# Kernel tuning notes

Measured on AMD Instinct MI355X. Metric: run time of the kernel, lower is better.

Reference implementation:

```python
import jax, jax.numpy as jnp
import numpy as np

THETA = 1.0       # spiking threshold (params['neuron']['theta'])
TAU_SR = 10.0     # SRM synaptic time constant (tauSr)
K = 100           # srm kernel support; alpha kernel has decayed to ~0 by 10*tau


def srm_kernel():
    # SLAYER SRMALPHA kernel: eps(t) = (t/tau) * exp(1 - t/tau), t = 0..K-1 (Ts = 1)
    t = jnp.arange(K, dtype=jnp.float32)
    return (t / TAU_SR) * jnp.exp(1.0 - t / TAU_SR)


def psp(x):
    # Causal temporal convolution with shared SRM kernel: y[t] = sum_s eps[s] * x[t-s]
    # x: [B, C, T]
    B, C, T = x.shape
    k = srm_kernel()[::-1].reshape(1, 1, K)  # flip: lax conv is correlation
    xr = x.reshape(B * C, 1, T)
    y = jax.lax.conv_general_dilated(xr, k, window_strides=(1,), padding=[(K - 1, 0)])
    return y.reshape(B, C, T)


def spike(u):
    # Hard threshold (forward of SLAYER spike function)
    return (u >= THETA).astype(u.dtype)


def setup_inputs() -> dict:
    key = jax.random.key(0)
    k1, k2, k3 = jax.random.split(key, 3)
    B, T = 256, 1000
    IN, HID, OUT = 78, 16, 20
    spike_input = (jax.random.uniform(k1, (B, IN, T)) < 0.1).astype(jnp.float32)
    W1 = jax.random.normal(k2, (HID, IN), dtype=jnp.float32) * 0.3
    W2 = jax.random.normal(k3, (OUT, HID), dtype=jnp.float32) * 0.3
    return {"spike_input": spike_input, "W1": W1, "W2": W2}


def reference(spike_input, W1, W2):
    # layer 1: dense (per-timestep matmul) -> psp temporal filter -> spike threshold
    u1 = psp(jnp.einsum('hi,bit->bht', W1, spike_input))  # [B, HID, T]
    s1 = spike(u1)
    # layer 2
    u2 = psp(jnp.einsum('oh,bht->bot', W2, s1))           # [B, OUT, T]
    return spike(u2)
```

## Files before the change

kernel.cpp:

```cpp
#include <hip/hip_runtime.h>
#include <math.h>


#define B_     256
#define IN_    78
#define HID_   16
#define OUT_   20
#define T_     1000
#define TT_    125
#define J_     224
#define ZSTR_  228
#define TC_    128
#define MSTR_  132

#define GRP(EP, A0,A1,A2,A3, B0,B1,B2,B3, C0,C1,C2) { \
  const double2 e01_ = *(const double2*)(EP); \
  const double2 e23_ = *(const double2*)((EP)+2); \
  u0 += e01_.x*(A3); u1 += e01_.x*(B0); u2 += e01_.x*(B1); u3 += e01_.x*(B2); \
  u4 += e01_.x*(B3); u5 += e01_.x*(C0); u6 += e01_.x*(C1); u7 += e01_.x*(C2); \
  u0 += e01_.y*(A2); u1 += e01_.y*(A3); u2 += e01_.y*(B0); u3 += e01_.y*(B1); \
  u4 += e01_.y*(B2); u5 += e01_.y*(B3); u6 += e01_.y*(C0); u7 += e01_.y*(C1); \
  u0 += e23_.x*(A1); u1 += e23_.x*(A2); u2 += e23_.x*(A3); u3 += e23_.x*(B0); \
  u4 += e23_.x*(B1); u5 += e23_.x*(B2); u6 += e23_.x*(B3); u7 += e23_.x*(C0); \
  u0 += e23_.y*(A0); u1 += e23_.y*(A1); u2 += e23_.y*(A2); u3 += e23_.y*(A3); \
  u4 += e23_.y*(B0); u5 += e23_.y*(B1); u6 += e23_.y*(B2); u7 += e23_.y*(B3); }

#define LOADF(X0,X1,X2,X3, P) { \
  const float4 lf_ = *(const float4*)(P); \
  X0 = (double)lf_.x; X1 = (double)lf_.y; X2 = (double)lf_.z; X3 = (double)lf_.w; }

__device__ __forceinline__ void init_eps_d(double* eps_d, int tid) {
  if (tid < 100) {
    float a = (float)tid / 10.0f;
    float e = a * expf(1.0f - a);
    eps_d[tid] = (double)e;
  }
}

#define MMROW2(XR, W0, W1) { \
  const float2 f0_ = *(const float2*)(XR); \
  const float2 f1_ = *(const float2*)((XR) + 64); \
  const double x0_=(double)f0_.x, x1_=(double)f0_.y; \
  const double x2_=(double)f1_.x, x3_=(double)f1_.y; \
  m00 += (W0)*x0_; m01 += (W0)*x1_; m02 += (W0)*x2_; m03 += (W0)*x3_; \
  m10 += (W1)*x0_; m11 += (W1)*x1_; m12 += (W1)*x2_; m13 += (W1)*x3_; }

#define STORE2(BASE, EOFF, MA, MB) \
  if (tb + (EOFF) < T_ - 1) \
    *(float2*)&zout[(BASE) + (size_t)(tb + (EOFF))] = \
        make_float2((float)(MA), (float)(MB));

__global__ __launch_bounds__(256) void mm1(
    const float* __restrict__ x, const float* __restrict__ W1,
    float* __restrict__ zout)
{
  __shared__ float  xs[13 * MSTR_];
  __shared__ double wd[16 * 80];

  const int tid = threadIdx.x;
  const int b   = blockIdx.x >> 3;
  const int tc  = blockIdx.x & 7;
  const int tcb = tc * TC_;

  for (int idx = tid; idx < HID_ * IN_; idx += 256)
    wd[(idx / IN_) * 80 + (idx % IN_)] = (double)W1[idx];

  const int  c_  = tid & 127;
  const int  r0_ = tid >> 7;
  const int  tg_ = tcb + c_;
  const bool tok = (tg_ < T_);
  const bool t6  = tok && (r0_ == 0);

  const int p = tid >> 5;
  const int q = tid & 31;

  double m00=0,m01=0,m02=0,m03=0,m10=0,m11=0,m12=0,m13=0;
  float g0,g1,g2,g3,g4,g5,g6;

#define ISSUE_MM1(CI) { \
    const float* xb_ = x + ((size_t)b * IN_ + (CI) * 13 + r0_) * T_ + tg_; \
    g0 = tok ? xb_[0]       : 0.0f; \
    g1 = tok ? xb_[2  * T_] : 0.0f; \
    g2 = tok ? xb_[4  * T_] : 0.0f; \
    g3 = tok ? xb_[6  * T_] : 0.0f; \
    g4 = tok ? xb_[8  * T_] : 0.0f; \
    g5 = tok ? xb_[10 * T_] : 0.0f; \
    g6 = t6  ? xb_[12 * T_] : 0.0f; }

  ISSUE_MM1(0)
  for (int ci = 0; ci < 6; ++ci) {
    __syncthreads();
    {
      float* dst = &xs[r0_ * MSTR_ + c_];
      dst[0]          = g0;  dst[2  * MSTR_] = g1;
      dst[4  * MSTR_] = g2;  dst[6  * MSTR_] = g3;
      dst[8  * MSTR_] = g4;  dst[10 * MSTR_] = g5;
      if (r0_ == 0) dst[12 * MSTR_] = g6;
    }
    __syncthreads();
    if (ci < 5) ISSUE_MM1(ci + 1)
    const int wbase0 = (2*p)     * 80 + ci * 13;
    const int wbase1 = (2*p + 1) * 80 + ci * 13;
#pragma unroll
    for (int i = 0; i < 13; ++i) {
      const float* xr = &xs[i * MSTR_ + 2 * q];
      MMROW2(xr, wd[wbase0 + i], wd[wbase1 + i])
    }
  }

  const size_t r0s = ((size_t)b * HID_ + 2*p) * T_;
  const size_t r1s = r0s + T_;
  const int tb = tcb + 2 * q;
  STORE2(r0s,  0, m00, m01)  STORE2(r0s, 64, m02, m03)
  STORE2(r1s,  0, m10, m11)  STORE2(r1s, 64, m12, m13)
}

__global__ __launch_bounds__(256) void mm2(
    const float* __restrict__ s1, const float* __restrict__ W2,
    float* __restrict__ zout)
{
  __shared__ float  ss[16 * MSTR_];
  __shared__ double wd[OUT_ * HID_];

  const int tid = threadIdx.x;
  const int b   = blockIdx.x >> 3;
  const int tc  = blockIdx.x & 7;
  const int tcb = tc * TC_;

  for (int idx = tid; idx < OUT_ * HID_; idx += 256)
    wd[idx] = (double)W2[idx];

  {
    const int  c_  = tid & 127;
    const int  r0_ = tid >> 7;
    const int  tg_ = tcb + c_;
    const bool tok = (tg_ < T_);
    const float* sb = s1 + ((size_t)b * HID_ + r0_) * T_ + tg_;
    float* dst = &ss[r0_ * MSTR_ + c_];
#pragma unroll
    for (int e = 0; e < 8; ++e)
      dst[2 * e * MSTR_] = tok ? sb[2 * e * T_] : 0.0f;
  }
  __syncthreads();

  const int p  = tid >> 5;
  const int q  = tid & 31;
  const int tb = tcb + 2 * q;

  for (int pg = p; pg < 10; pg += 8) {
    double m00=0,m01=0,m02=0,m03=0,m10=0,m11=0,m12=0,m13=0;
    const int wbase0 = (2*pg)     * HID_;
    const int wbase1 = (2*pg + 1) * HID_;
#pragma unroll
    for (int i = 0; i < HID_; ++i) {
      const float* xr = &ss[i * MSTR_ + 2 * q];
      MMROW2(xr, wd[wbase0 + i], wd[wbase1 + i])
    }
    const size_t r0s = ((size_t)b * OUT_ + 2*pg) * T_;
    const size_t r1s = r0s + T_;
    STORE2(r0s,  0, m00, m01)  STORE2(r0s, 64, m02, m03)
    STORE2(r1s,  0, m10, m11)  STORE2(r1s, 64, m12, m13)
  }
}

__global__ __launch_bounds__(256) void fir_g(
    const float* __restrict__ zin, float* __restrict__ sout,
    int R, int tile_fixed)
{
  __shared__ float zf[OUT_ * ZSTR_];
  __shared__ __align__(16) double eps_d[100];

  const int tid  = threadIdx.x;
  const int b    = (tile_fixed >= 0) ? (int)blockIdx.x : (int)(blockIdx.x >> 3);
  const int tile = (tile_fixed >= 0) ? tile_fixed      : (int)(blockIdx.x & 7);
  const int t0   = tile * TT_;

  init_eps_d(eps_d, tid);
  for (int idx = tid; idx < R * ZSTR_; idx += 256) {
    const int cc = idx % ZSTR_;
    const int t  = t0 - 99 + cc;
    const int r  = idx / ZSTR_;
    zf[idx] = (cc < J_ && t >= 0) ? zin[((size_t)b * R + r) * T_ + t] : 0.0f;
  }
  __syncthreads();

  for (int task = tid; task < R * 16; task += 256) {
    const int h = task >> 4, q = task & 15;
    const float* zrow = &zf[h * ZSTR_ + 8 * q];
    double u0=0,u1=0,u2=0,u3=0,u4=0,u5=0,u6=0,u7=0;
    double A0,A1,A2,A3,B0,B1,B2,B3,C0,C1,C2,C3;
    LOADF(A0,A1,A2,A3, zrow + 96);
    LOADF(B0,B1,B2,B3, zrow + 100);
    LOADF(C0,C1,C2,C3, zrow + 104);
    GRP(eps_d, A0,A1,A2,A3, B0,B1,B2,B3, C0,C1,C2)

    const float*  zp = zrow + 92;
    const double* ep = eps_d + 4;
#pragma unroll 1
    for (int k = 0; k < 8; ++k) {
      LOADF(C0,C1,C2,C3, zp);
      GRP(ep,     C0,C1,C2,C3, A0,A1,A2,A3, B0,B1,B2)
      LOADF(B0,B1,B2,B3, zp - 4);
      GRP(ep + 4, B0,B1,B2,B3, C0,C1,C2,C3, A0,A1,A2)
      LOADF(A0,A1,A2,A3, zp - 8);
      GRP(ep + 8, A0,A1,A2,A3, B0,B1,B2,B3, C0,C1,C2)
      zp -= 12; ep += 12;
    }

    const size_t base = ((size_t)b * R + h) * T_ + t0 + 8 * q;
    const int tb = 8 * q;
    const float f0=(float)u0, f1=(float)u1, f2=(float)u2, f3=(float)u3;
    const float f4=(float)u4, f5=(float)u5, f6=(float)u6, f7=(float)u7;
    sout[base + 0] = (f0 >= 1.0f) ? 1.0f : 0.0f;
    sout[base + 1] = (f1 >= 1.0f) ? 1.0f : 0.0f;
    sout[base + 2] = (f2 >= 1.0f) ? 1.0f : 0.0f;
    sout[base + 3] = (f3 >= 1.0f) ? 1.0f : 0.0f;
    if (tb + 4 < TT_) sout[base + 4] = (f4 >= 1.0f) ? 1.0f : 0.0f;
    if (tb + 5 < TT_) sout[base + 5] = (f5 >= 1.0f) ? 1.0f : 0.0f;
    if (tb + 6 < TT_) sout[base + 6] = (f6 >= 1.0f) ? 1.0f : 0.0f;
    if (tb + 7 < TT_) sout[base + 7] = (f7 >= 1.0f) ? 1.0f : 0.0f;
  }
}

extern "C" void kernel_launch(void* const* d_in, const int* in_sizes, int n_in,
                              void* d_out, int out_size, void* d_ws, size_t ws_size,
                              hipStream_t stream) {
  const float* x  = (const float*)d_in[0];
  const float* W1 = (const float*)d_in[1];
  const float* W2 = (const float*)d_in[2];
  float* outp = (float*)d_out;
  float* base = (float*)d_ws;

  const size_t Z1E = (size_t)B_ * HID_ * T_;
  const size_t Z2E = (size_t)B_ * OUT_ * T_;

  if (ws_size >= (Z1E + Z2E) * sizeof(float)) {
    float* z1 = base;
    float* s1 = base + Z2E;
    float* z2 = base;
    mm1<<<dim3(B_ * 8), dim3(256), 0, stream>>>(x, W1, z1);
    fir_g<<<dim3(B_ * 8), dim3(256), 0, stream>>>(z1, s1, HID_, -1);
    mm2<<<dim3(B_ * 8), dim3(256), 0, stream>>>(s1, W2, z2);
    fir_g<<<dim3(B_ * 8), dim3(256), 0, stream>>>(z2, outp, OUT_, -1);
  } else if (ws_size >= 2 * Z1E * sizeof(float)) {
    float* z1 = base;
    float* s1 = base + Z1E;
    mm1<<<dim3(B_ * 8), dim3(256), 0, stream>>>(x, W1, z1);
    fir_g<<<dim3(B_ * 8), dim3(256), 0, stream>>>(z1, s1, HID_, -1);
    mm2<<<dim3(B_ * 8), dim3(256), 0, stream>>>(s1, W2, outp);
    for (int k = 7; k >= 0; --k)
      fir_g<<<dim3(B_), dim3(256), 0, stream>>>(outp, outp, OUT_, k);
  } else {
    float* z1 = base;
    mm1<<<dim3(B_ * 8), dim3(256), 0, stream>>>(x, W1, z1);
    for (int k = 7; k >= 0; --k)
      fir_g<<<dim3(B_), dim3(256), 0, stream>>>(z1, z1, HID_, k);
    mm2<<<dim3(B_ * 8), dim3(256), 0, stream>>>(z1, W2, outp);
    for (int k = 7; k >= 0; --k)
      fir_g<<<dim3(B_), dim3(256), 0, stream>>>(outp, outp, OUT_, k);
  }
}
```

Before: 109.8 us.

## Fuse layer-1 FIR/threshold with layer-2 matmul into one kernel

Adds a kernel that loads a z1 time tile with halo into shared memory, runs the first PSP filter and threshold, keeps the s1 spikes in shared memory, and immediately does the W2 matmul to write z2. This removes one kernel launch and the global round trip of s1. The final FIR now runs with 320 threads so all 20 output rows times 16 tasks are covered in one pass, and z1 is staged in the output buffer to reduce workspace needs. The fused kernel carries larger shared memory, which may reduce occupancy.

```diff
diff --git a/kernel.cpp b/kernel.cpp
--- a/kernel.cpp
+++ b/kernel.cpp
@@ -28,6 +28,25 @@
 #define LOADF(X0,X1,X2,X3, P) { \
   const float4 lf_ = *(const float4*)(P); \
   X0 = (double)lf_.x; X1 = (double)lf_.y; X2 = (double)lf_.z; X3 = (double)lf_.w; }
+
+#define FIR_BODY(ZROW) { \
+  double A0,A1,A2,A3,B0,B1,B2,B3,C0,C1,C2,C3; \
+  LOADF(A0,A1,A2,A3, (ZROW) + 96); \
+  LOADF(B0,B1,B2,B3, (ZROW) + 100); \
+  LOADF(C0,C1,C2,C3, (ZROW) + 104); \
+  GRP(eps_d, A0,A1,A2,A3, B0,B1,B2,B3, C0,C1,C2) \
+  const float*  zp_ = (ZROW) + 92; \
+  const double* ep_ = eps_d + 4; \
+  _Pragma("unroll 1") \
+  for (int k_ = 0; k_ < 8; ++k_) { \
+    LOADF(C0,C1,C2,C3, zp_); \
+    GRP(ep_,     C0,C1,C2,C3, A0,A1,A2,A3, B0,B1,B2) \
+    LOADF(B0,B1,B2,B3, zp_ - 4); \
+    GRP(ep_ + 4, B0,B1,B2,B3, C0,C1,C2,C3, A0,A1,A2) \
+    LOADF(A0,A1,A2,A3, zp_ - 8); \
+    GRP(ep_ + 8, A0,A1,A2,A3, B0,B1,B2,B3, C0,C1,C2) \
+    zp_ -= 12; ep_ += 12; \
+  } }
 
 __device__ __forceinline__ void init_eps_d(double* eps_d, int tid) {
   if (tid < 100) {
@@ -115,55 +134,79 @@
   STORE2(r1s,  0, m10, m11)  STORE2(r1s, 64, m12, m13)
 }
 
-__global__ __launch_bounds__(256) void mm2(
-    const float* __restrict__ s1, const float* __restrict__ W2,
-    float* __restrict__ zout)
+__global__ __launch_bounds__(256) void fm(
+    const float* __restrict__ z1, const float* __restrict__ W2,
+    float* __restrict__ z2)
 {
-  __shared__ float  ss[16 * MSTR_];
-  __shared__ double wd[OUT_ * HID_];
-
-  const int tid = threadIdx.x;
-  const int b   = blockIdx.x >> 3;
-  const int tc  = blockIdx.x & 7;
-  const int tcb = tc * TC_;
-
+  __shared__ float zf[HID_ * ZSTR_];
+  __shared__ float sf[HID_ * 128];
+  __shared__ float wf[OUT_ * HID_];
+  __shared__ __align__(16) double eps_d[100];
+
+  const int tid  = threadIdx.x;
+  const int b    = blockIdx.x >> 3;
+  const int tile = blockIdx.x & 7;
+  const int t0   = tile * TT_;
+
+  init_eps_d(eps_d, tid);
   for (int idx = tid; idx < OUT_ * HID_; idx += 256)
-    wd[idx] = (double)W2[idx];
+    wf[idx] = W2[idx];
+  for (int idx = tid; idx < HID_ * ZSTR_; idx += 256) {
+    const int cc = idx % ZSTR_;
+    const int t  = t0 - 99 + cc;
+    const int r  = idx / ZSTR_;
+    zf[idx] = (cc < J_ && t >= 0) ? z1[((size_t)b * HID_ + r) * T_ + t] : 0.0f;
+  }
+  __syncthreads();
 
   {
-    const int  c_  = tid & 127;
-    const int  r0_ = tid >> 7;
-    const int  tg_ = tcb + c_;
-    const bool tok = (tg_ < T_);
-    const float* sb = s1 + ((size_t)b * HID_ + r0_) * T_ + tg_;
-    float* dst = &ss[r0_ * MSTR_ + c_];
+    const int h = tid >> 4, q16 = tid & 15;
+    const float* zrow = &zf[h * ZSTR_ + 8 * q16];
+    double u0=0,u1=0,u2=0,u3=0,u4=0,u5=0,u6=0,u7=0;
+    FIR_BODY(zrow)
+    float* sd = &sf[h * 128 + 8 * q16];
+    sd[0] = ((float)u0 >= 1.0f) ? 1.0f : 0.0f;
+    sd[1] = ((float)u1 >= 1.0f) ? 1.0f : 0.0f;
+    sd[2] = ((float)u2 >= 1.0f) ? 1.0f : 0.0f;
+    sd[3] = ((float)u3 >= 1.0f) ? 1.0f : 0.0f;
+    sd[4] = ((float)u4 >= 1.0f) ? 1.0f : 0.0f;
+    sd[5] = ((float)u5 >= 1.0f) ? 1.0f : 0.0f;
+    sd[6] = ((float)u6 >= 1.0f) ? 1.0f : 0.0f;
+    sd[7] = ((float)u7 >= 1.0f) ? 1.0f : 0.0f;
+  }
+  __syncthreads();
+
+  {
+    const int p = tid >> 5;
+    const int q = tid & 31;
+#pragma unroll 1
+    for (int pg = p; pg < 10; pg += 8) {
+      double m00=0,m01=0,m02=0,m03=0,m10=0,m11=0,m12=0,m13=0;
+      const int wb0 = (2*pg)     * HID_;
+      const int wb1 = (2*pg + 1) * HID_;
 #pragma unroll
-    for (int e = 0; e < 8; ++e)
-      dst[2 * e * MSTR_] = tok ? sb[2 * e * T_] : 0.0f;
-  }
-  __syncthreads();
-
-  const int p  = tid >> 5;
-  const int q  = tid & 31;
-  const int tb = tcb + 2 * q;
-
-  for (int pg = p; pg < 10; pg += 8) {
-    double m00=0,m01=0,m02=0,m03=0,m10=0,m11=0,m12=0,m13=0;
-    const int wbase0 = (2*pg)     * HID_;
-    const int wbase1 = (2*pg + 1) * HID_;
-#pragma unroll
-    for (int i = 0; i < HID_; ++i) {
-      const float* xr = &ss[i * MSTR_ + 2 * q];
-      MMROW2(xr, wd[wbase0 + i], wd[wbase1 + i])
+      for (int i = 0; i < HID_; ++i) {
+        const float* xr = &sf[i * 128 + 2 * q];
+        MMROW2(xr, (double)wf[wb0 + i], (double)wf[wb1 + i])
+      }
+      const size_t r0s = ((size_t)b * OUT_ + 2*pg) * T_ + t0;
+      const size_t r1s = r0s + T_;
+      const int c0 = 2 * q;
+      *(float2*)&z2[r0s + c0] = make_float2((float)m00, (float)m01);
+      *(float2*)&z2[r1s + c0] = make_float2((float)m10, (float)m11);
+      const int c1 = 64 + 2 * q;
+      if (c1 + 1 < TT_) {
+        *(float2*)&z2[r0s + c1] = make_float2((float)m02, (float)m03);
+        *(float2*)&z2[r1s + c1] = make_float2((float)m12, (float)m13);
+      } else if (c1 < TT_) {
+        z2[r0s + c1] = (float)m02;
+        z2[r1s + c1] = (float)m12;
+      }
     }
-    const size_t r0s = ((size_t)b * OUT_ + 2*pg) * T_;
-    const size_t r1s = r0s + T_;
-    STORE2(r0s,  0, m00, m01)  STORE2(r0s, 64, m02, m03)
-    STORE2(r1s,  0, m10, m11)  STORE2(r1s, 64, m12, m13)
-  }
-}
-
-__global__ __launch_bounds__(256) void fir_g(
+  }
+}
+
+__global__ __launch_bounds__(320) void fir_g(
     const float* __restrict__ zin, float* __restrict__ sout,
     int R, int tile_fixed)
 {
@@ -171,12 +214,13 @@
   __shared__ __align__(16) double eps_d[100];
 
   const int tid  = threadIdx.x;
+  const int nthr = blockDim.x;
   const int b    = (tile_fixed >= 0) ? (int)blockIdx.x : (int)(blockIdx.x >> 3);
   const int tile = (tile_fixed >= 0) ? tile_fixed      : (int)(blockIdx.x & 7);
   const int t0   = tile * TT_;
 
   init_eps_d(eps_d, tid);
-  for (int idx = tid; idx < R * ZSTR_; idx += 256) {
+  for (int idx = tid; idx < R * ZSTR_; idx += nthr) {
     const int cc = idx % ZSTR_;
     const int t  = t0 - 99 + cc;
     const int r  = idx / ZSTR_;
@@ -184,31 +228,13 @@
   }
   __syncthreads();
 
-  for (int task = tid; task < R * 16; task += 256) {
-    const int h = task >> 4, q = task & 15;
-    const float* zrow = &zf[h * ZSTR_ + 8 * q];
+  for (int task = tid; task < R * 16; task += nthr) {
+    const int h = task >> 4, q16 = task & 15;
+    const float* zrow = &zf[h * ZSTR_ + 8 * q16];
     double u0=0,u1=0,u2=0,u3=0,u4=0,u5=0,u6=0,u7=0;
-    double A0,A1,A2,A3,B0,B1,B2,B3,C0,C1,C2,C3;
-    LOADF(A0,A1,A2,A3, zrow + 96);
-    LOADF(B0,B1,B2,B3, zrow + 100);
-    LOADF(C0,C1,C2,C3, zrow + 104);
-    GRP(eps_d, A0,A1,A2,A3, B0,B1,B2,B3, C0,C1,C2)
-
-    const float*  zp = zrow + 92;
-    const double* ep = eps_d + 4;
-#pragma unroll 1
-    for (int k = 0; k < 8; ++k) {
-      LOADF(C0,C1,C2,C3, zp);
-      GRP(ep,     C0,C1,C2,C3, A0,A1,A2,A3, B0,B1,B2)
-      LOADF(B0,B1,B2,B3, zp - 4);
-      GRP(ep + 4, B0,B1,B2,B3, C0,C1,C2,C3, A0,A1,A2)
-      LOADF(A0,A1,A2,A3, zp - 8);
-      GRP(ep + 8, A0,A1,A2,A3, B0,B1,B2,B3, C0,C1,C2)
-      zp -= 12; ep += 12;
-    }
-
-    const size_t base = ((size_t)b * R + h) * T_ + t0 + 8 * q;
-    const int tb = 8 * q;
+    FIR_BODY(zrow)
+    const size_t base = ((size_t)b * R + h) * T_ + t0 + 8 * q16;
+    const int tb = 8 * q16;
     const float f0=(float)u0, f1=(float)u1, f2=(float)u2, f3=(float)u3;
     const float f4=(float)u4, f5=(float)u5, f6=(float)u6, f7=(float)u7;
     sout[base + 0] = (f0 >= 1.0f) ? 1.0f : 0.0f;
@@ -231,32 +257,20 @@
   float* outp = (float*)d_out;
   float* base = (float*)d_ws;
 
-  const size_t Z1E = (size_t)B_ * HID_ * T_;
   const size_t Z2E = (size_t)B_ * OUT_ * T_;
 
-  if (ws_size >= (Z1E + Z2E) * sizeof(float)) {
-    float* z1 = base;
-    float* s1 = base + Z2E;
+  if (ws_size >= Z2E * sizeof(float)) {
+    float* z1 = outp;
     float* z2 = base;
-    mm1<<<dim3(B_ * 8), dim3(256), 0, stream>>>(x, W1, z1);
-    fir_g<<<dim3(B_ * 8), dim3(256), 0, stream>>>(z1, s1, HID_, -1);
-    mm2<<<dim3(B_ * 8), dim3(256), 0, stream>>>(s1, W2, z2);
-    fir_g<<<dim3(B_ * 8), dim3(256), 0, stream>>>(z2, outp, OUT_, -1);
-  } else if (ws_size >= 2 * Z1E * sizeof(float)) {
-    float* z1 = base;
-    float* s1 = base + Z1E;
-    mm1<<<dim3(B_ * 8), dim3(256), 0, stream>>>(x, W1, z1);
-    fir_g<<<dim3(B_ * 8), dim3(256), 0, stream>>>(z1, s1, HID_, -1);
-    mm2<<<dim3(B_ * 8), dim3(256), 0, stream>>>(s1, W2, outp);
-    for (int k = 7; k >= 0; --k)
-      fir_g<<<dim3(B_), dim3(256), 0, stream>>>(outp, outp, OUT_, k);
+    mm1  <<<dim3(B_ * 8), dim3(256), 0, stream>>>(x,  W1, z1);
+    fm   <<<dim3(B_ * 8), dim3(256), 0, stream>>>(z1, W2, z2);
+    fir_g<<<dim3(B_ * 8), dim3(320), 0, stream>>>(z2, outp, OUT_, -1);
   } else {
     float* z1 = base;
-    mm1<<<dim3(B_ * 8), dim3(256), 0, stream>>>(x, W1, z1);
+    float* z2 = outp;
+    mm1<<<dim3(B_ * 8), dim3(256), 0, stream>>>(x,  W1, z1);
+    fm <<<dim3(B_ * 8), dim3(256), 0, stream>>>(z1, W2, z2);
     for (int k = 7; k >= 0; --k)
-      fir_g<<<dim3(B_), dim3(256), 0, stream>>>(z1, z1, HID_, k);
-    mm2<<<dim3(B_ * 8), dim3(256), 0, stream>>>(z1, W2, outp);
-    for (int k = 7; k >= 0; --k)
-      fir_g<<<dim3(B_), dim3(256), 0, stream>>>(outp, outp, OUT_, k);
-  }
-}
+      fir_g<<<dim3(B_), dim3(320), 0, stream>>>(z2, z2, OUT_, k);
+  }
+}
```

New measurement: 115.4 us. +5.1%, slower.
